# Kernel tuning notes

Hardware: AMD Instinct MI355X
Metric: run time of the kernel (lower is better)

## Reference

```python
import jax, jax.numpy as jnp
import numpy as np

N_POINTS = 1048576
N_LEVELS = 16
F = 2
BASE_RES = 16
FINEST_RES = 512
LOG2_HASH = 19
SIZES = [2 ** min(i + 1, LOG2_HASH) for i in range(N_LEVELS)]  # per-level table rows (powers of 2)
OFFS = np.concatenate([[0], np.cumsum(SIZES)]).astype(np.int64)  # static row offsets into packed table
TOTAL_ROWS = int(OFFS[-1])  # 131070
# hash primes from the torch module; uint32 wraparound matches int64 low-bit behavior
# because each table size is a power of two <= 2^19 < 2^32, so h % 2^k == low k bits.
P0, P1, P2, P3 = np.uint32(1), np.uint32(2654435761), np.uint32(29675113), np.uint32(123456789)
CORNERS = np.array([[0,0,0],[1,0,0],[0,1,0],[1,1,0],
                    [0,0,1],[1,0,1],[0,1,1],[1,1,1]], dtype=np.uint32)  # torch stacking order


def setup_inputs() -> dict:
    key = jax.random.key(0)
    k1, k2 = jax.random.split(key)
    coords = jax.random.uniform(k1, (N_POINTS, 3), dtype=jnp.float32, minval=-1.0, maxval=1.0)
    hash_init_scale = 0.001
    table = jax.random.uniform(k2, (TOTAL_ROWS, F), dtype=jnp.float32,
                               minval=-hash_init_scale, maxval=hash_init_scale)
    return {"coords": coords, "table": table}


def _encode(coords, table):
    corners = jnp.asarray(CORNERS)  # [8,3] uint32
    outs = []
    for level in range(N_LEVELS):
        res = min(BASE_RES * (2 ** level), FINEST_RES)
        cs = (coords + 1.0) * res           # [N,3]
        cf = jnp.floor(cs)
        frac = cs - cf                      # [N,3]
        base = cf.astype(jnp.uint32)        # coords >= -1 so floor >= 0
        c = base[None, :, :] + corners[:, None, :]   # [8,N,3]
        x, y, z = c[..., 0], c[..., 1], c[..., 2]
        h = x * P0
        h = h * P1 + y
        h = h * P2 + z
        h = h * P3
        h = (h & jnp.uint32(SIZES[level] - 1)).astype(jnp.int32)  # mod power-of-2 table size
        feats = table[int(OFFS[level]) + h]          # [8,N,F] gather
        tx = frac[..., 0:1]; ty = frac[..., 1:2]; tz = frac[..., 2:3]
        f = (feats[0] * (1 - tx) * (1 - ty) * (1 - tz)
             + feats[1] * tx * (1 - ty) * (1 - tz)
             + feats[2] * (1 - tx) * ty * (1 - tz)
             + feats[3] * tx * ty * (1 - tz)
             + feats[4] * (1 - tx) * (1 - ty) * tz
             + feats[5] * tx * (1 - ty) * tz
             + feats[6] * (1 - tx) * ty * tz
             + feats[7] * tx * ty * tz)              # [N,F]
        outs.append(f)
    return jnp.concatenate(outs, axis=-1)            # [N, N_LEVELS*F]


def reference(coords, table):
    return _encode(coords, table)
```

## Files before the change

### kernel.cpp

```cpp
#include <hip/hip_runtime.h>
#include <hip/hip_fp16.h>


#define BLOCK 1024
#define NBLOCKS 512
#define ITERS 16
#define TBL_ROWS 16382
#define TBL_LDS_BYTES 131072
#define LDS_BYTES (TBL_LDS_BYTES + 16 * 128 * 8)

constexpr unsigned P1 = 2654435761u, P2 = 29675113u, P3 = 123456789u;
constexpr unsigned HA = P1 * P2 * P3;
constexpr unsigned HB = P2 * P3;
constexpr unsigned HC = P3;

#define PREP3(FRES, H3, WARR) \
    unsigned H3[8]; float WARR[8]; { \
        const float csx = (px + 1.0f) * (FRES); \
        const float csy = (py + 1.0f) * (FRES); \
        const float csz = (pz + 1.0f) * (FRES); \
        const float cfx = floorf(csx), cfy = floorf(csy), cfz = floorf(csz); \
        const float tx = csx - cfx, ty = csy - cfy, tz = csz - cfz; \
        const unsigned hh = ((unsigned)cfx * HA + (unsigned)cfy * HB + (unsigned)cfz * HC) << 3; \
        const float ux = 1.0f - tx, uy = 1.0f - ty, uz = 1.0f - tz; \
        const float m00 = uy * uz, m10 = ty * uz, m01 = uy * tz, m11 = ty * tz; \
        WARR[0] = ux * m00; WARR[1] = tx * m00; \
        WARR[2] = ux * m10; WARR[3] = tx * m10; \
        WARR[4] = ux * m01; WARR[5] = tx * m01; \
        WARR[6] = ux * m11; WARR[7] = tx * m11; \
        H3[0] = hh;                        H3[1] = hh + (HA << 3); \
        H3[2] = hh + (HB << 3);            H3[3] = hh + ((HA + HB) << 3); \
        H3[4] = hh + (HC << 3);            H3[5] = hh + ((HA + HC) << 3); \
        H3[6] = hh + ((HB + HC) << 3);     H3[7] = hh + ((HA + HB + HC) << 3); \
    }

template<int LA, int LB, bool GB>
__device__ __forceinline__ void computePair(
    const char* ldsb, const float* __restrict__ table,
    float px, float py, float pz, float2& oA, float2& oB)
{
    constexpr unsigned MA8 = ((2u << LA) - 1u) << 3;
    constexpr unsigned OA8 = ((2u << LA) - 2u) << 3;
    constexpr unsigned MB8 = ((2u << LB) - 1u) << 3;
    constexpr unsigned OB8 = ((2u << LB) - 2u) << 3;

    float a0 = 0.0f, a1 = 0.0f, b0 = 0.0f, b1 = 0.0f;

    if constexpr (GB) {
        PREP3(512.0f, h3B, wB)
        const char* gb = (const char*)table + OB8;
        const float2 g0 = *(const float2*)(gb + (h3B[0] & MB8));
        const float2 g1 = *(const float2*)(gb + (h3B[1] & MB8));
        const float2 g2 = *(const float2*)(gb + (h3B[2] & MB8));
        const float2 g3 = *(const float2*)(gb + (h3B[3] & MB8));
        const float2 g4 = *(const float2*)(gb + (h3B[4] & MB8));
        const float2 g5 = *(const float2*)(gb + (h3B[5] & MB8));
        const float2 g6 = *(const float2*)(gb + (h3B[6] & MB8));
        const float2 g7 = *(const float2*)(gb + (h3B[7] & MB8));
        {
            PREP3((float)(16 << LA), h3A, wA)
#pragma unroll
            for (int c = 0; c < 8; ++c) {
                float2 f = *(const float2*)(ldsb + OA8 + (h3A[c] & MA8));
                a0 += f.x * wA[c]; a1 += f.y * wA[c];
            }
        }
        b0 += g0.x * wB[0]; b1 += g0.y * wB[0];
        b0 += g1.x * wB[1]; b1 += g1.y * wB[1];
        b0 += g2.x * wB[2]; b1 += g2.y * wB[2];
        b0 += g3.x * wB[3]; b1 += g3.y * wB[3];
        b0 += g4.x * wB[4]; b1 += g4.y * wB[4];
        b0 += g5.x * wB[5]; b1 += g5.y * wB[5];
        b0 += g6.x * wB[6]; b1 += g6.y * wB[6];
        b0 += g7.x * wB[7]; b1 += g7.y * wB[7];
    } else if constexpr (LA >= 5) {
        PREP3(512.0f, h3, w)
#pragma unroll
        for (int c = 0; c < 8; ++c) {
            float2 f = *(const float2*)(ldsb + OA8 + (h3[c] & MA8));
            a0 += f.x * w[c]; a1 += f.y * w[c];
        }
#pragma unroll
        for (int c = 0; c < 8; ++c) {
            float2 f = *(const float2*)(ldsb + OB8 + (h3[c] & MB8));
            b0 += f.x * w[c]; b1 += f.y * w[c];
        }
    } else {
        {
            PREP3((float)(16 << LA), h3A, wA)
#pragma unroll
            for (int c = 0; c < 8; ++c) {
                float2 f = *(const float2*)(ldsb + OA8 + (h3A[c] & MA8));
                a0 += f.x * wA[c]; a1 += f.y * wA[c];
            }
        }
        {
            PREP3(512.0f, h3B, wB)
#pragma unroll
            for (int c = 0; c < 8; ++c) {
                float2 f = *(const float2*)(ldsb + OB8 + (h3B[c] & MB8));
                b0 += f.x * wB[c]; b1 += f.y * wB[c];
            }
        }
    }
    oA = make_float2(a0, a1);
    oB = make_float2(b0, b1);
}

__global__ __launch_bounds__(BLOCK) void ngp_encode_kernel(
    const float* __restrict__ coords,
    const float* __restrict__ table,
    float* __restrict__ out)
{
    extern __shared__ unsigned char lds_raw[];
    const char* ldsb = (const char*)lds_raw;
    float2* lds_t = (float2*)(lds_raw + TBL_LDS_BYTES);

    {
        const float4* __restrict__ t4 = (const float4*)table;
        float4* __restrict__ l4 = (float4*)lds_raw;
        for (int r = threadIdx.x; r < TBL_ROWS / 2; r += BLOCK)
            l4[r] = t4[r];
    }
    __syncthreads();

    const float2* __restrict__ tbf = (const float2*)table;
    (void)tbf;
    float4* __restrict__ out4 = (float4*)out;

    const int wv   = __builtin_amdgcn_readfirstlane((int)(threadIdx.x >> 6));
    const int q    = wv & 7;
    const int g    = wv >> 3;
    const int lane = threadIdx.x & 63;
    const int pl   = g * 64 + lane;

    const int lA = q;
    const int lB = 15 - q;
    const unsigned xA = (unsigned)(lA & 14), xB = (unsigned)(lB & 14);

    for (int it = 0; it < ITERS; ++it) {
        const int pbase = blockIdx.x * (ITERS * 128) + it * 128;
        const int p = pbase + pl;

        const float px = coords[3 * p + 0];
        const float py = coords[3 * p + 1];
        const float pz = coords[3 * p + 2];

        float2 oA, oB;
        switch (q) {
        case 0: computePair<0, 15, true >(ldsb, table, px, py, pz, oA, oB); break;
        case 1: computePair<1, 14, true >(ldsb, table, px, py, pz, oA, oB); break;
        case 2: computePair<2, 13, true >(ldsb, table, px, py, pz, oA, oB); break;
        case 3: computePair<3, 12, false>(ldsb, table, px, py, pz, oA, oB); break;
        case 4: computePair<4, 11, false>(ldsb, table, px, py, pz, oA, oB); break;
        case 5: computePair<5, 10, false>(ldsb, table, px, py, pz, oA, oB); break;
        case 6: computePair<6,  9, false>(ldsb, table, px, py, pz, oA, oB); break;
        default: computePair<7, 8, false>(ldsb, table, px, py, pz, oA, oB); break;
        }

        lds_t[lA * 128 + (pl ^ xA)] = oA;
        lds_t[lB * 128 + (pl ^ xB)] = oB;
        __syncthreads();
        {
            const int j  = threadIdx.x;
            const int lp = j >> 3, qq = j & 7;
            float2 a = lds_t[(2 * qq + 0) * 128 + (lp ^ (2 * qq))];
            float2 b = lds_t[(2 * qq + 1) * 128 + (lp ^ (2 * qq))];
            out4[(size_t)pbase * 8 + j] = make_float4(a.x, a.y, b.x, b.y);
        }
        __syncthreads();
    }
}

extern "C" void kernel_launch(void* const* d_in, const int* in_sizes, int n_in,
                              void* d_out, int out_size, void* d_ws, size_t ws_size,
                              hipStream_t stream) {
    const float* coords = (const float*)d_in[0];
    const float* table  = (const float*)d_in[1];
    float* out = (float*)d_out;

    hipFuncSetAttribute((const void*)ngp_encode_kernel,
                        hipFuncAttributeMaxDynamicSharedMemorySize,
                        LDS_BYTES);

    ngp_encode_kernel<<<NBLOCKS, BLOCK, LDS_BYTES, stream>>>(coords, table, out);
}
```

Before: 248.7 us.

## Stage LDS hash table in fp16 and prefetch next iteration coords

```diff
diff --git a/kernel.cpp b/kernel.cpp
--- a/kernel.cpp
+++ b/kernel.cpp
@@ -5,14 +5,34 @@
 #define BLOCK 1024
 #define NBLOCKS 512
 #define ITERS 16
-#define TBL_ROWS 16382
-#define TBL_LDS_BYTES 131072
+#define STAGED_ROWS 16382
+#define TBL_LDS_BYTES 65536
 #define LDS_BYTES (TBL_LDS_BYTES + 16 * 128 * 8)
 
 constexpr unsigned P1 = 2654435761u, P2 = 29675113u, P3 = 123456789u;
 constexpr unsigned HA = P1 * P2 * P3;
 constexpr unsigned HB = P2 * P3;
 constexpr unsigned HC = P3;
+
+#define PREP2(FRES, H2, WARR) \
+    unsigned H2[8]; float WARR[8]; { \
+        const float csx = (px + 1.0f) * (FRES); \
+        const float csy = (py + 1.0f) * (FRES); \
+        const float csz = (pz + 1.0f) * (FRES); \
+        const float cfx = floorf(csx), cfy = floorf(csy), cfz = floorf(csz); \
+        const float tx = csx - cfx, ty = csy - cfy, tz = csz - cfz; \
+        const unsigned hh = ((unsigned)cfx * HA + (unsigned)cfy * HB + (unsigned)cfz * HC) << 2; \
+        const float ux = 1.0f - tx, uy = 1.0f - ty, uz = 1.0f - tz; \
+        const float m00 = uy * uz, m10 = ty * uz, m01 = uy * tz, m11 = ty * tz; \
+        WARR[0] = ux * m00; WARR[1] = tx * m00; \
+        WARR[2] = ux * m10; WARR[3] = tx * m10; \
+        WARR[4] = ux * m01; WARR[5] = tx * m01; \
+        WARR[6] = ux * m11; WARR[7] = tx * m11; \
+        H2[0] = hh;                        H2[1] = hh + (HA << 2); \
+        H2[2] = hh + (HB << 2);            H2[3] = hh + ((HA + HB) << 2); \
+        H2[4] = hh + (HC << 2);            H2[5] = hh + ((HA + HC) << 2); \
+        H2[6] = hh + ((HB + HC) << 2);     H2[7] = hh + ((HA + HB + HC) << 2); \
+    }
 
 #define PREP3(FRES, H3, WARR) \
     unsigned H3[8]; float WARR[8]; { \
@@ -34,34 +54,41 @@
         H3[6] = hh + ((HB + HC) << 3);     H3[7] = hh + ((HA + HB + HC) << 3); \
     }
 
+__device__ __forceinline__ float2 h2f(unsigned u) {
+    __half2 hh = *(__half2*)&u;
+    return __half22float2(hh);
+}
+
 template<int LA, int LB, bool GB>
 __device__ __forceinline__ void computePair(
-    const char* ldsb, const float* __restrict__ table,
+    const char* ldsc, const char* gtab,
     float px, float py, float pz, float2& oA, float2& oB)
 {
-    constexpr unsigned MA8 = ((2u << LA) - 1u) << 3;
-    constexpr unsigned OA8 = ((2u << LA) - 2u) << 3;
-    constexpr unsigned MB8 = ((2u << LB) - 1u) << 3;
-    constexpr unsigned OB8 = ((2u << LB) - 2u) << 3;
+    constexpr unsigned MA2 = ((2u << LA) - 1u) << 2;
+    constexpr unsigned OA2 = ((2u << LA) - 2u) << 2;
+    constexpr unsigned MB2 = ((2u << LB) - 1u) << 2;
+    constexpr unsigned OB2 = ((2u << LB) - 2u) << 2;
+    constexpr unsigned MB3 = ((2u << LB) - 1u) << 3;
+    constexpr unsigned OB3 = ((2u << LB) - 2u) << 3;
 
     float a0 = 0.0f, a1 = 0.0f, b0 = 0.0f, b1 = 0.0f;
 
     if constexpr (GB) {
         PREP3(512.0f, h3B, wB)
-        const char* gb = (const char*)table + OB8;
-        const float2 g0 = *(const float2*)(gb + (h3B[0] & MB8));
-        const float2 g1 = *(const float2*)(gb + (h3B[1] & MB8));
-        const float2 g2 = *(const float2*)(gb + (h3B[2] & MB8));
-        const float2 g3 = *(const float2*)(gb + (h3B[3] & MB8));
-        const float2 g4 = *(const float2*)(gb + (h3B[4] & MB8));
-        const float2 g5 = *(const float2*)(gb + (h3B[5] & MB8));
-        const float2 g6 = *(const float2*)(gb + (h3B[6] & MB8));
-        const float2 g7 = *(const float2*)(gb + (h3B[7] & MB8));
-        {
-            PREP3((float)(16 << LA), h3A, wA)
+        const char* gb = gtab + OB3;
+        const float2 g0 = *(const float2*)(gb + (h3B[0] & MB3));
+        const float2 g1 = *(const float2*)(gb + (h3B[1] & MB3));
+        const float2 g2 = *(const float2*)(gb + (h3B[2] & MB3));
+        const float2 g3 = *(const float2*)(gb + (h3B[3] & MB3));
+        const float2 g4 = *(const float2*)(gb + (h3B[4] & MB3));
+        const float2 g5 = *(const float2*)(gb + (h3B[5] & MB3));
+        const float2 g6 = *(const float2*)(gb + (h3B[6] & MB3));
+        const float2 g7 = *(const float2*)(gb + (h3B[7] & MB3));
+        {
+            PREP2((float)(16 << LA), h2A, wA)
 #pragma unroll
             for (int c = 0; c < 8; ++c) {
-                float2 f = *(const float2*)(ldsb + OA8 + (h3A[c] & MA8));
+                float2 f = h2f(*(const unsigned*)(ldsc + OA2 + (h2A[c] & MA2)));
                 a0 += f.x * wA[c]; a1 += f.y * wA[c];
             }
         }
@@ -74,31 +101,31 @@
         b0 += g6.x * wB[6]; b1 += g6.y * wB[6];
         b0 += g7.x * wB[7]; b1 += g7.y * wB[7];
     } else if constexpr (LA >= 5) {
-        PREP3(512.0f, h3, w)
+        PREP2(512.0f, h2, w)
 #pragma unroll
         for (int c = 0; c < 8; ++c) {
-            float2 f = *(const float2*)(ldsb + OA8 + (h3[c] & MA8));
+            float2 f = h2f(*(const unsigned*)(ldsc + OA2 + (h2[c] & MA2)));
             a0 += f.x * w[c]; a1 += f.y * w[c];
         }
 #pragma unroll
         for (int c = 0; c < 8; ++c) {
-            float2 f = *(const float2*)(ldsb + OB8 + (h3[c] & MB8));
+            float2 f = h2f(*(const unsigned*)(ldsc + OB2 + (h2[c] & MB2)));
             b0 += f.x * w[c]; b1 += f.y * w[c];
         }
     } else {
         {
-            PREP3((float)(16 << LA), h3A, wA)
+            PREP2((float)(16 << LA), h2A, wA)
 #pragma unroll
             for (int c = 0; c < 8; ++c) {
-                float2 f = *(const float2*)(ldsb + OA8 + (h3A[c] & MA8));
+                float2 f = h2f(*(const unsigned*)(ldsc + OA2 + (h2A[c] & MA2)));
                 a0 += f.x * wA[c]; a1 += f.y * wA[c];
             }
         }
         {
-            PREP3(512.0f, h3B, wB)
+            PREP2(512.0f, h2B, wB)
 #pragma unroll
             for (int c = 0; c < 8; ++c) {
-                float2 f = *(const float2*)(ldsb + OB8 + (h3B[c] & MB8));
+                float2 f = h2f(*(const unsigned*)(ldsc + OB2 + (h2B[c] & MB2)));
                 b0 += f.x * wB[c]; b1 += f.y * wB[c];
             }
         }
@@ -113,19 +140,25 @@
     float* __restrict__ out)
 {
     extern __shared__ unsigned char lds_raw[];
-    const char* ldsb = (const char*)lds_raw;
+    const char* ldsc = (const char*)lds_raw;
     float2* lds_t = (float2*)(lds_raw + TBL_LDS_BYTES);
 
     {
         const float4* __restrict__ t4 = (const float4*)table;
-        float4* __restrict__ l4 = (float4*)lds_raw;
-        for (int r = threadIdx.x; r < TBL_ROWS / 2; r += BLOCK)
-            l4[r] = t4[r];
+        uint2* __restrict__ l2 = (uint2*)lds_raw;
+        for (int r = threadIdx.x; r < STAGED_ROWS / 2; r += BLOCK) {
+            float4 v = t4[r];
+            __half2 a = __floats2half2_rn(v.x, v.y);
+            __half2 b = __floats2half2_rn(v.z, v.w);
+            uint2 u;
+            u.x = *(unsigned*)&a;
+            u.y = *(unsigned*)&b;
+            l2[r] = u;
+        }
     }
     __syncthreads();
 
-    const float2* __restrict__ tbf = (const float2*)table;
-    (void)tbf;
+    const char* gtab = (const char*)table;
     float4* __restrict__ out4 = (float4*)out;
 
     const int wv   = __builtin_amdgcn_readfirstlane((int)(threadIdx.x >> 6));
@@ -138,24 +171,33 @@
     const int lB = 15 - q;
     const unsigned xA = (unsigned)(lA & 14), xB = (unsigned)(lB & 14);
 
+    int p0 = blockIdx.x * (ITERS * 128) + pl;
+    float cx = coords[3 * p0 + 0];
+    float cy = coords[3 * p0 + 1];
+    float cz = coords[3 * p0 + 2];
+
     for (int it = 0; it < ITERS; ++it) {
         const int pbase = blockIdx.x * (ITERS * 128) + it * 128;
-        const int p = pbase + pl;
-
-        const float px = coords[3 * p + 0];
-        const float py = coords[3 * p + 1];
-        const float pz = coords[3 * p + 2];
+
+        const float px = cx, py = cy, pz = cz;
+
+        if (it + 1 < ITERS) {
+            const int pn = pbase + 128 + pl;
+            cx = coords[3 * pn + 0];
+            cy = coords[3 * pn + 1];
+            cz = coords[3 * pn + 2];
+        }
 
         float2 oA, oB;
         switch (q) {
-        case 0: computePair<0, 15, true >(ldsb, table, px, py, pz, oA, oB); break;
-        case 1: computePair<1, 14, true >(ldsb, table, px, py, pz, oA, oB); break;
-        case 2: computePair<2, 13, true >(ldsb, table, px, py, pz, oA, oB); break;
-        case 3: computePair<3, 12, false>(ldsb, table, px, py, pz, oA, oB); break;
-        case 4: computePair<4, 11, false>(ldsb, table, px, py, pz, oA, oB); break;
-        case 5: computePair<5, 10, false>(ldsb, table, px, py, pz, oA, oB); break;
-        case 6: computePair<6,  9, false>(ldsb, table, px, py, pz, oA, oB); break;
-        default: computePair<7, 8, false>(ldsb, table, px, py, pz, oA, oB); break;
+        case 0: computePair<0, 15, true >(ldsc, gtab, px, py, pz, oA, oB); break;
+        case 1: computePair<1, 14, true >(ldsc, gtab, px, py, pz, oA, oB); break;
+        case 2: computePair<2, 13, true >(ldsc, gtab, px, py, pz, oA, oB); break;
+        case 3: computePair<3, 12, false>(ldsc, gtab, px, py, pz, oA, oB); break;
+        case 4: computePair<4, 11, false>(ldsc, gtab, px, py, pz, oA, oB); break;
+        case 5: computePair<5, 10, false>(ldsc, gtab, px, py, pz, oA, oB); break;
+        case 6: computePair<6,  9, false>(ldsc, gtab, px, py, pz, oA, oB); break;
+        default: computePair<7, 8, false>(ldsc, gtab, px, py, pz, oA, oB); break;
         }
 
         lds_t[lA * 128 + (pl ^ xA)] = oA;
```

Measured after the change: 229.2 us. 1.08x faster.
